# Kernel tuning notes

Hardware: AMD Instinct MI355X
Metric: run time of the kernel (lower is better)

## Reference

```python
import jax, jax.numpy as jnp
import numpy as np

EMB = 1024
HEADS = 16
EPS = 1e-6


def setup_inputs() -> dict:
    key = jax.random.key(0)
    ks = jax.random.split(key, 12)
    B, S, D = 2, 2048, EMB
    scale = 1.0 / np.sqrt(D)
    inp = {
        "v": jax.random.normal(ks[0], (B, S, D), jnp.float32),
        "k": jax.random.normal(ks[1], (B, S, D), jnp.float32),
        "q": jax.random.normal(ks[2], (B, S, D), jnp.float32),
        "Wv": jax.random.normal(ks[3], (D, D), jnp.float32) * scale,
        "bv": jnp.zeros((D,), jnp.float32),
        "Wk": jax.random.normal(ks[4], (D, D), jnp.float32) * scale,
        "bk": jnp.zeros((D,), jnp.float32),
        "Wq": jax.random.normal(ks[5], (D, D), jnp.float32) * scale,
        "bq": jnp.zeros((D,), jnp.float32),
        "Wo": jax.random.normal(ks[6], (D, D), jnp.float32) * scale,
        "bo": jnp.zeros((D,), jnp.float32),
        "gamma": jnp.ones((D,), jnp.float32),
        "beta": jnp.zeros((D,), jnp.float32),
    }
    return inp


def reference(v, k, q, Wv, bv, Wk, bk, Wq, bq, Wo, bo, gamma, beta):
    B, S, D = q.shape
    H = HEADS
    d = D // H  # head depth

    def split_heads(x):  # [B,S,D] -> [B,H,S,d]
        return x.reshape(B, S, H, d).transpose(0, 2, 1, 3)

    V = split_heads(v @ Wv + bv)
    K = split_heads(k @ Wk + bk)
    Q = split_heads(q @ Wq + bq)

    # scaled dot-product attention (full score matrix, no mask)
    scores = jnp.einsum("bhqd,bhkd->bhqk", Q, K) / jnp.sqrt(jnp.float32(d))
    attn = jax.nn.softmax(scores, axis=-1)
    ctx = jnp.einsum("bhqk,bhkd->bhqd", attn, V)

    ctx = ctx.transpose(0, 2, 1, 3).reshape(B, S, D)
    out = ctx @ Wo + bo + q  # final dense + residual

    # LayerNormalization(epsilon=1e-6) over last axis
    mu = jnp.mean(out, axis=-1, keepdims=True)
    var = jnp.var(out, axis=-1, keepdims=True)
    return gamma * (out - mu) * jax.lax.rsqrt(var + EPS) + beta
```

## Files before the change

kernel.cpp:

```cpp
#include <hip/hip_runtime.h>
#include <hip/hip_bf16.h>
#include <math.h>

#define D_EMB 1024
#define NBATCH 2
#define SEQ 2048
#define NH 16
#define HDIM 64
#define MTOT (NBATCH*SEQ)
#define NT (SEQ/64)

typedef unsigned short u16;
typedef __attribute__((ext_vector_type(8))) short bf16x8;
typedef __attribute__((ext_vector_type(4))) float f32x4;
typedef __attribute__((ext_vector_type(16))) float f32x16;
typedef __attribute__((ext_vector_type(4))) unsigned short u16x4;
typedef __attribute__((ext_vector_type(4))) unsigned int u32x4;

__device__ __forceinline__ u16 f2b(float f) {
  union { float f; unsigned u; } x; x.f = f;
  unsigned r = x.u + 0x7fffu + ((x.u >> 16) & 1u);
  return (u16)(r >> 16);
}
__device__ __forceinline__ float b2f(u16 u) {
  union { unsigned u; float f; } x; x.u = ((unsigned)u) << 16;
  return x.f;
}

__device__ __forceinline__ void gld_lds16(const u16* g, u16* l) {
  __builtin_amdgcn_global_load_lds(
      (const __attribute__((address_space(1))) void*)g,
      (__attribute__((address_space(3))) void*)l, 16, 0, 0);
}

__global__ __launch_bounds__(256) void convert_qkv(
    const float* __restrict__ v, const float* __restrict__ k, const float* __restrict__ q,
    u16* __restrict__ vb, u16* __restrict__ kb, u16* __restrict__ qb) {
  int idx = blockIdx.x * 256 + threadIdx.x;
  float4 a;
  u16x4 o;
  a = ((const float4*)v)[idx];
  o.x = f2b(a.x); o.y = f2b(a.y); o.z = f2b(a.z); o.w = f2b(a.w);
  ((u16x4*)vb)[idx] = o;
  a = ((const float4*)k)[idx];
  o.x = f2b(a.x); o.y = f2b(a.y); o.z = f2b(a.z); o.w = f2b(a.w);
  ((u16x4*)kb)[idx] = o;
  a = ((const float4*)q)[idx];
  o.x = f2b(a.x); o.y = f2b(a.y); o.z = f2b(a.z); o.w = f2b(a.w);
  ((u16x4*)qb)[idx] = o;
}

__global__ __launch_bounds__(256) void transpose_w(
    const float* __restrict__ Wv, const float* __restrict__ Wk,
    const float* __restrict__ Wq, const float* __restrict__ Wo,
    u16* __restrict__ Wvt, u16* __restrict__ Wkt,
    u16* __restrict__ Wqt, u16* __restrict__ Wot) {
  __shared__ float tile[32][33];
  int z = blockIdx.z;
  const float* W = (z==0) ? Wv : (z==1) ? Wk : (z==2) ? Wq : Wo;
  u16* Wt = (z==0) ? Wvt : (z==1) ? Wkt : (z==2) ? Wqt : Wot;
  int tx = threadIdx.x, ty = threadIdx.y;
  int n0 = blockIdx.x * 32, k0 = blockIdx.y * 32;
#pragma unroll
  for (int i = 0; i < 4; ++i)
    tile[ty + i*8][tx] = W[(size_t)(k0 + ty + i*8) * D_EMB + n0 + tx];
  __syncthreads();
#pragma unroll
  for (int i = 0; i < 4; ++i)
    Wt[(size_t)(n0 + ty + i*8) * D_EMB + k0 + tx] = f2b(tile[tx][ty + i*8]);
}

__global__ __launch_bounds__(256) void transpose_v(
    const u16* __restrict__ Vh, u16* __restrict__ Vt) {
  __shared__ u16 t[64][65];
  const int bhx = blockIdx.y, s0 = blockIdx.x * 64;
  const int tid = threadIdx.x;
  const u16* src = Vh + ((size_t)bhx * SEQ + s0) * HDIM;
  const int r = tid >> 3, seg = (tid & 7) * 8;
  bf16x8 a0 = *(const bf16x8*)(src + (size_t)r * HDIM + seg);
  bf16x8 a1 = *(const bf16x8*)(src + (size_t)(r + 32) * HDIM + seg);
#pragma unroll
  for (int j = 0; j < 8; ++j) {
    t[r][seg + j] = (u16)a0[j];
    t[r + 32][seg + j] = (u16)a1[j];
  }
  __syncthreads();
  const int dd = tid >> 3, ss = (tid & 7) * 8;
  bf16x8 w0, w1;
#pragma unroll
  for (int j = 0; j < 8; ++j) {
    w0[j] = (short)t[ss + j][dd];
    w1[j] = (short)t[ss + j][dd + 32];
  }
  *(bf16x8*)(Vt + ((size_t)bhx * HDIM + dd) * SEQ + s0 + ss) = w0;
  *(bf16x8*)(Vt + ((size_t)bhx * HDIM + dd + 32) * SEQ + s0 + ss) = w1;
}

__device__ __forceinline__ void gemm_loop(
    const u16* __restrict__ A, const u16* __restrict__ Bt,
    u16* lds_a, u16* lds_b, int bm, int bn, int wid, int lane,
    int wr, int wc, f32x4 acc[4][4]) {
#pragma unroll 1
  for (int kt = 0; kt < D_EMB/64; ++kt) {
    __syncthreads();
#pragma unroll
    for (int i = 0; i < 4; ++i) {
      int chunk = i*4 + wid;
      int row = chunk*8 + (lane >> 3);
      int slot = (lane & 7) ^ (row & 7);
      const u16* srcA = A + (size_t)(bm*128 + row) * D_EMB + kt*64 + slot*8;
      gld_lds16(srcA, lds_a + chunk*512);
      const u16* srcB = Bt + (size_t)(bn*128 + row) * D_EMB + kt*64 + slot*8;
      gld_lds16(srcB, lds_b + chunk*512);
    }
    __syncthreads();
#pragma unroll
    for (int st = 0; st < 2; ++st) {
      bf16x8 af[4], bfr[4];
#pragma unroll
      for (int mb = 0; mb < 4; ++mb) {
        int row = wr*64 + mb*16 + (lane & 15);
        int slot = (st*4 + (lane >> 4)) ^ (row & 7);
        af[mb] = *(const bf16x8*)(lds_a + row*64 + slot*8);
      }
#pragma unroll
      for (int nb = 0; nb < 4; ++nb) {
        int row = wc*64 + nb*16 + (lane & 15);
        int slot = (st*4 + (lane >> 4)) ^ (row & 7);
        bfr[nb] = *(const bf16x8*)(lds_b + row*64 + slot*8);
      }
#pragma unroll
      for (int mb = 0; mb < 4; ++mb)
#pragma unroll
        for (int nb = 0; nb < 4; ++nb)
          acc[mb][nb] = __builtin_amdgcn_mfma_f32_16x16x32_bf16(af[mb], bfr[nb], acc[mb][nb], 0, 0, 0);
    }
  }
}

__global__ __launch_bounds__(256) void gemm_qkv(
    const u16* __restrict__ vb, const u16* __restrict__ kb, const u16* __restrict__ qb,
    const u16* __restrict__ Wvt, const u16* __restrict__ Wkt, const u16* __restrict__ Wqt,
    const float* __restrict__ bv, const float* __restrict__ bk, const float* __restrict__ bq,
    u16* __restrict__ Vh, u16* __restrict__ Kh, u16* __restrict__ Qh) {
  __shared__ u16 lds_a[128*64];
  __shared__ u16 lds_b[128*64];
  int z = blockIdx.z;
  const u16* A  = (z==0) ? vb : (z==1) ? kb : qb;
  const u16* Bt = (z==0) ? Wvt : (z==1) ? Wkt : Wqt;
  const float* bias = (z==0) ? bv : (z==1) ? bk : bq;
  u16* Out = (z==0) ? Vh : (z==1) ? Kh : Qh;
  int tid = threadIdx.x, wid = tid >> 6, lane = tid & 63;
  int wr = wid >> 1, wc = wid & 1;
  int bm = blockIdx.y, bn = blockIdx.x;
  f32x4 acc[4][4];
#pragma unroll
  for (int i = 0; i < 4; ++i)
#pragma unroll
    for (int j = 0; j < 4; ++j) acc[i][j] = (f32x4){0.f,0.f,0.f,0.f};
  gemm_loop(A, Bt, lds_a, lds_b, bm, bn, wid, lane, wr, wc, acc);
  int g = lane >> 4, c = lane & 15;
  const float scl = (z == 2) ? 0.18033688f : 1.0f;
#pragma unroll
  for (int mb = 0; mb < 4; ++mb) {
    int row0 = bm*128 + wr*64 + mb*16 + g*4;
#pragma unroll
    for (int nb = 0; nb < 4; ++nb) {
      int col = bn*128 + wc*64 + nb*16 + c;
      float bsv = bias[col];
      int h = col >> 6, dd = col & 63;
#pragma unroll
      for (int r = 0; r < 4; ++r) {
        int m = row0 + r; int b = m >> 11, s = m & (SEQ-1);
        Out[(((size_t)b*NH + h)*SEQ + s)*HDIM + dd] = f2b((acc[mb][nb][r] + bsv) * scl);
      }
    }
  }
}

__global__ __launch_bounds__(256, 2) void attn_k(
    const u16* __restrict__ Qh, const u16* __restrict__ Kh,
    const u16* __restrict__ Vt, u16* __restrict__ ctx) {
  __shared__ u16 kt_lds[4][64*64];
  __shared__ u16 vt_lds[4][64*64];
  const int tid = threadIdx.x, wid = tid >> 6, lane = tid & 63;
  const int lo5 = lane & 31, hi = lane >> 5;
  const int bid = blockIdx.x;
  const int xcd = bid & 7, idx = bid >> 3;
  const int qblk = idx & 15, bhg = idx >> 4;
  const int bh = bhg * 8 + xcd;
  const int qb = qblk * 128 + wid * 32;
  const size_t base = (size_t)bh * SEQ * HDIM;

  const int srow = tid >> 3;
  const int c0 = (tid & 7) ^ (srow & 7) ^ (srow >> 3);
  const int c1 = c0 ^ 4;
  const u16* kp0 = Kh + base + (size_t)srow * HDIM + c0*8;
  const u16* kp1 = Kh + base + (size_t)(srow+32) * HDIM + c1*8;
  const u16* vp0 = Vt + base + (size_t)srow * SEQ + c0*8;
  const u16* vp1 = Vt + base + (size_t)(srow+32) * SEQ + c1*8;

  const int r7 = lo5 & 7, r3 = lo5 >> 3;
  int offs0[4], offs1[4];
#pragma unroll
  for (int t = 0; t < 4; ++t) {
    int p = (2*t + hi) ^ r7 ^ r3;
    offs0[t] = lo5*128 + p*16;
    offs1[t] = (lo5+32)*128 + (p^4)*16;
  }
  const char* ktbase = (const char*)&kt_lds[0][0];
  const char* vtbase = (const char*)&vt_lds[0][0];

  bf16x8 qf[4];
#pragma unroll
  for (int t = 0; t < 4; ++t)
    qf[t] = *(const bf16x8*)(Qh + base + (size_t)(qb + lo5)*HDIM + t*16 + hi*8);

  f32x16 z16;
#pragma unroll
  for (int i = 0; i < 16; ++i) z16[i] = 0.f;

  f32x16 o0, o1;
#pragma unroll
  for (int i = 0; i < 16; ++i) { o0[i] = 0.f; o1[i] = 0.f; }
  float lsum = 0.f;

#define STAGE(B) do { \
    gld_lds16(kp0, &kt_lds[B][wid*512]); \
    gld_lds16(kp1, &kt_lds[B][2048 + wid*512]); \
    gld_lds16(vp0, &vt_lds[B][wid*512]); \
    gld_lds16(vp1, &vt_lds[B][2048 + wid*512]); \
    kp0 += 64*HDIM; kp1 += 64*HDIM; vp0 += 64; vp1 += 64; \
  } while (0)

#define TILE(B, VMSTR, DOSTAGE, SB) do { \
    asm volatile("s_waitcnt " VMSTR ::: "memory"); \
    __builtin_amdgcn_sched_barrier(0); \
    __builtin_amdgcn_s_barrier();             \
    __builtin_amdgcn_sched_barrier(0); \
    const char* kb_ = ktbase + (B)*8192; \
    const char* vb_ = vtbase + (B)*8192; \
    bf16x8 kf0[4], kf1[4], vf0[4], vf1[4]; \
    _Pragma("unroll") for (int t = 0; t < 4; ++t) { \
      kf0[t] = *(const bf16x8*)(kb_ + offs0[t]); \
      kf1[t] = *(const bf16x8*)(kb_ + offs1[t]); \
      vf0[t] = *(const bf16x8*)(vb_ + offs0[t]); \
      vf1[t] = *(const bf16x8*)(vb_ + offs1[t]); } \
    if (DOSTAGE) { STAGE(SB); } \
    __builtin_amdgcn_sched_barrier(0); \
    __builtin_amdgcn_s_setprio(1); \
    f32x16 st0 = __builtin_amdgcn_mfma_f32_32x32x16_bf16(kf0[0], qf[0], z16, 0, 0, 0); \
    f32x16 st1 = __builtin_amdgcn_mfma_f32_32x32x16_bf16(kf1[0], qf[0], z16, 0, 0, 0); \
    _Pragma("unroll") for (int t = 1; t < 4; ++t) { \
      st0 = __builtin_amdgcn_mfma_f32_32x32x16_bf16(kf0[t], qf[t], st0, 0, 0, 0); \
      st1 = __builtin_amdgcn_mfma_f32_32x32x16_bf16(kf1[t], qf[t], st1, 0, 0, 0); } \
    __builtin_amdgcn_s_setprio(0); \
    _Pragma("unroll") for (int r = 0; r < 16; ++r) { \
      st0[r] = exp2f(st0[r]); st1[r] = exp2f(st1[r]); } \
    float ps = st0[0] + st0[1]; \
    _Pragma("unroll") for (int r = 2; r < 16; ++r) ps += st0[r]; \
    _Pragma("unroll") for (int r = 0; r < 16; ++r) ps += st1[r]; \
    lsum += ps; \
    bf16x8 pa[4]; \
    _Pragma("unroll") for (int ks = 0; ks < 2; ++ks) { \
      const f32x16& s_ = ks ? st1 : st0; \
      unsigned X[8]; \
      _Pragma("unroll") for (int w = 0; w < 8; ++w) { \
        float lo_f = s_[2*w], hi_f = s_[2*w + 1]; \
        asm("v_cvt_pk_bf16_f32 %0, %1, %2" : "=v"(X[w]) : "v"(lo_f), "v"(hi_f)); } \
      asm volatile("v_permlane32_swap_b32 %0, %1" : "+v"(X[0]), "+v"(X[2])); \
      asm volatile("v_permlane32_swap_b32 %0, %1" : "+v"(X[1]), "+v"(X[3])); \
      asm volatile("v_permlane32_swap_b32 %0, %1" : "+v"(X[4]), "+v"(X[6])); \
      asm volatile("v_permlane32_swap_b32 %0, %1" : "+v"(X[5]), "+v"(X[7])); \
      union { u32x4 u; bf16x8 b; } cva, cvb; \
      cva.u = (u32x4){X[0], X[1], X[2], X[3]}; \
      cvb.u = (u32x4){X[4], X[5], X[6], X[7]}; \
      pa[2*ks]   = cva.b; \
      pa[2*ks+1] = cvb.b; } \
    __builtin_amdgcn_s_setprio(1); \
    _Pragma("unroll") for (int t = 0; t < 4; ++t) { \
      o0 = __builtin_amdgcn_mfma_f32_32x32x16_bf16(pa[t], vf0[t], o0, 0, 0, 0); \
      o1 = __builtin_amdgcn_mfma_f32_32x32x16_bf16(pa[t], vf1[t], o1, 0, 0, 0); } \
    __builtin_amdgcn_s_setprio(0); \
  } while (0)

  STAGE(0);
  STAGE(1);

#pragma unroll 1
  for (int kv = 0; kv < NT - 4; kv += 4) {
    TILE(0, "vmcnt(4)", 1, 2);
    TILE(1, "vmcnt(4)", 1, 3);
    TILE(2, "vmcnt(4)", 1, 0);
    TILE(3, "vmcnt(4)", 1, 1);
  }
  TILE(0, "vmcnt(4)", 1, 2);
  TILE(1, "vmcnt(4)", 1, 3);
  TILE(2, "vmcnt(4)", 0, 0);
  TILE(3, "vmcnt(0)", 0, 0);

#undef STAGE
#undef TILE

  lsum += __shfl_xor(lsum, 32);
  float linv = 1.0f / lsum;
  const int b = bh >> 4, h = bh & 15;
#pragma unroll
  for (int r = 0; r < 16; ++r) {
    int crow = (r & 3) + 8*(r >> 2) + 4*hi;
    float lr = __int_as_float(
        __builtin_amdgcn_ds_bpermute(crow << 2, __float_as_int(linv)));
    int s = qb + crow;
    u16* row = ctx + ((size_t)(b*SEQ + s))*D_EMB + h*64;
    row[lo5]      = f2b(o0[r] * lr);
    row[32 + lo5] = f2b(o1[r] * lr);
  }
}

__global__ __launch_bounds__(256) void gemm_out(
    const u16* __restrict__ ctx, const u16* __restrict__ Wot,
    const float* __restrict__ bo, const u16* __restrict__ resid,
    u16* __restrict__ preln) {
  __shared__ u16 lds_a[128*64];
  __shared__ u16 lds_b[128*64];
  int tid = threadIdx.x, wid = tid >> 6, lane = tid & 63;
  int wr = wid >> 1, wc = wid & 1;
  int bm = blockIdx.y, bn = blockIdx.x;
  f32x4 acc[4][4];
#pragma unroll
  for (int i = 0; i < 4; ++i)
#pragma unroll
    for (int j = 0; j < 4; ++j) acc[i][j] = (f32x4){0.f,0.f,0.f,0.f};
  gemm_loop(ctx, Wot, lds_a, lds_b, bm, bn, wid, lane, wr, wc, acc);
  int g = lane >> 4, c = lane & 15;
#pragma unroll
  for (int mb = 0; mb < 4; ++mb) {
    int row0 = bm*128 + wr*64 + mb*16 + g*4;
#pragma unroll
    for (int nb = 0; nb < 4; ++nb) {
      int col = bn*128 + wc*64 + nb*16 + c;
      float bsv = bo[col];
#pragma unroll
      for (int r = 0; r < 4; ++r) {
        int m = row0 + r;
        float v = acc[mb][nb][r] + bsv + b2f(resid[(size_t)m*D_EMB + col]);
        preln[(size_t)m*D_EMB + col] = f2b(v);
      }
    }
  }
}

__global__ __launch_bounds__(256) void ln_k(
    const u16* __restrict__ preln, const float* __restrict__ gamma,
    const float* __restrict__ beta, float* __restrict__ out) {
  int row = blockIdx.x, tid = threadIdx.x;
  u16x4 xr = ((const u16x4*)(preln + (size_t)row*D_EMB))[tid];
  float x0 = b2f(xr.x), x1 = b2f(xr.y), x2 = b2f(xr.z), x3 = b2f(xr.w);
  float s  = x0 + x1 + x2 + x3;
  float ss = x0*x0 + x1*x1 + x2*x2 + x3*x3;
#pragma unroll
  for (int off = 32; off; off >>= 1) {
    s  += __shfl_xor(s, off);
    ss += __shfl_xor(ss, off);
  }
  __shared__ float red_s[4], red_ss[4];
  int wid = tid >> 6, lane = tid & 63;
  if (lane == 0) { red_s[wid] = s; red_ss[wid] = ss; }
  __syncthreads();
  s  = red_s[0] + red_s[1] + red_s[2] + red_s[3];
  ss = red_ss[0] + red_ss[1] + red_ss[2] + red_ss[3];
  float mu = s * (1.0f/1024.0f);
  float var = ss * (1.0f/1024.0f) - mu*mu;
  float rstd = rsqrtf(var + 1e-6f);
  float4 gm = ((const float4*)gamma)[tid];
  float4 bt = ((const float4*)beta)[tid];
  float4 y;
  y.x = (x0 - mu)*rstd*gm.x + bt.x;
  y.y = (x1 - mu)*rstd*gm.y + bt.y;
  y.z = (x2 - mu)*rstd*gm.z + bt.z;
  y.w = (x3 - mu)*rstd*gm.w + bt.w;
  ((float4*)(out + (size_t)row*D_EMB))[tid] = y;
}

extern "C" void kernel_launch(void* const* d_in, const int* in_sizes, int n_in,
                              void* d_out, int out_size, void* d_ws, size_t ws_size,
                              hipStream_t stream) {
  const float* v_in  = (const float*)d_in[0];
  const float* k_in  = (const float*)d_in[1];
  const float* q_in  = (const float*)d_in[2];
  const float* Wv    = (const float*)d_in[3];
  const float* bv    = (const float*)d_in[4];
  const float* Wk    = (const float*)d_in[5];
  const float* bk    = (const float*)d_in[6];
  const float* Wq    = (const float*)d_in[7];
  const float* bq    = (const float*)d_in[8];
  const float* Wo    = (const float*)d_in[9];
  const float* bo    = (const float*)d_in[10];
  const float* gamma = (const float*)d_in[11];
  const float* beta  = (const float*)d_in[12];
  char* ws = (char*)d_ws;

  const size_t TOKB = (size_t)MTOT * D_EMB * 2;
  const size_t WB   = (size_t)D_EMB * D_EMB * 2;
  size_t o_qb = 0;
  size_t o_kb = o_qb + TOKB;
  size_t o_vb = o_kb + TOKB;
  size_t o_wq = o_vb + TOKB;
  size_t o_wk = o_wq + WB;
  size_t o_wv = o_wk + WB;
  size_t o_wo = o_wv + WB;
  size_t o_Qh = o_wo + WB;
  size_t o_Kh = o_Qh + TOKB;
  size_t o_Vt = o_Kh + TOKB;
  size_t o_cx = o_Vt + TOKB;

  u16* qb  = (u16*)(ws + o_qb);
  u16* kb  = (u16*)(ws + o_kb);
  u16* vb  = (u16*)(ws + o_vb);
  u16* wqt = (u16*)(ws + o_wq);
  u16* wkt = (u16*)(ws + o_wk);
  u16* wvt = (u16*)(ws + o_wv);
  u16* wot = (u16*)(ws + o_wo);
  u16* Qh  = (u16*)(ws + o_Qh);
  u16* Kh  = (u16*)(ws + o_Kh);
  u16* Vt  = (u16*)(ws + o_Vt);
  u16* cx  = (u16*)(ws + o_cx);
  u16* Vh  = cx;
  u16* preln = vb;

  convert_qkv<<<4096, 256, 0, stream>>>(v_in, k_in, q_in, vb, kb, qb);
  transpose_w<<<dim3(32, 32, 4), dim3(32, 8), 0, stream>>>(Wv, Wk, Wq, Wo, wvt, wkt, wqt, wot);
  gemm_qkv<<<dim3(8, 32, 3), 256, 0, stream>>>(vb, kb, qb, wvt, wkt, wqt, bv, bk, bq, Vh, Kh, Qh);
  transpose_v<<<dim3(32, 32), 256, 0, stream>>>(Vh, Vt);
  attn_k<<<512, 256, 0, stream>>>(Qh, Kh, Vt, cx);
  gemm_out<<<dim3(8, 32), 256, 0, stream>>>(cx, wot, bo, qb, preln);
  ln_k<<<4096, 256, 0, stream>>>(preln, gamma, beta, (float*)d_out);
}
```

Before: 155.4 us.

## Shrink GEMM M-tile to 64 rows and double-buffer attention K/V staging

The QKV and output projection GEMMs now use 64x128 block tiles instead of 128x128, which doubles the grid (8x64 blocks) to fill more compute units, at the cost of less operand reuse per block. The attention kernel's K/V LDS ring shrinks from four buffers to two. A second barrier after each tile's LDS reads lets the next tile's prefetch overwrite the same buffer. This halves LDS use, which may help occupancy, but it adds a barrier per tile and leaves less prefetch depth to hide memory latency.

```diff
diff --git a/kernel.cpp b/kernel.cpp
--- a/kernel.cpp
+++ b/kernel.cpp
@@ -96,43 +96,49 @@
   *(bf16x8*)(Vt + ((size_t)bhx * HDIM + dd + 32) * SEQ + s0 + ss) = w1;
 }
 
-__device__ __forceinline__ void gemm_loop(
+__device__ __forceinline__ void gemm_loop64(
     const u16* __restrict__ A, const u16* __restrict__ Bt,
     u16* lds_a, u16* lds_b, int bm, int bn, int wid, int lane,
-    int wr, int wc, f32x4 acc[4][4]) {
+    f32x4 acc[4][2]) {
 #pragma unroll 1
   for (int kt = 0; kt < D_EMB/64; ++kt) {
     __syncthreads();
+#pragma unroll
+    for (int i = 0; i < 2; ++i) {
+      int chunk = wid*2 + i;
+      int row = chunk*8 + (lane >> 3);
+      int slot = (lane & 7) ^ (row & 7);
+      gld_lds16(A + (size_t)(bm*64 + row) * D_EMB + kt*64 + slot*8,
+                lds_a + chunk*512);
+    }
 #pragma unroll
     for (int i = 0; i < 4; ++i) {
       int chunk = i*4 + wid;
       int row = chunk*8 + (lane >> 3);
       int slot = (lane & 7) ^ (row & 7);
-      const u16* srcA = A + (size_t)(bm*128 + row) * D_EMB + kt*64 + slot*8;
-      gld_lds16(srcA, lds_a + chunk*512);
-      const u16* srcB = Bt + (size_t)(bn*128 + row) * D_EMB + kt*64 + slot*8;
-      gld_lds16(srcB, lds_b + chunk*512);
+      gld_lds16(Bt + (size_t)(bn*128 + row) * D_EMB + kt*64 + slot*8,
+                lds_b + chunk*512);
     }
     __syncthreads();
 #pragma unroll
     for (int st = 0; st < 2; ++st) {
-      bf16x8 af[4], bfr[4];
+      bf16x8 af[4], bfr[2];
 #pragma unroll
       for (int mb = 0; mb < 4; ++mb) {
-        int row = wr*64 + mb*16 + (lane & 15);
+        int row = mb*16 + (lane & 15);
         int slot = (st*4 + (lane >> 4)) ^ (row & 7);
         af[mb] = *(const bf16x8*)(lds_a + row*64 + slot*8);
       }
 #pragma unroll
-      for (int nb = 0; nb < 4; ++nb) {
-        int row = wc*64 + nb*16 + (lane & 15);
+      for (int nb = 0; nb < 2; ++nb) {
+        int row = wid*32 + nb*16 + (lane & 15);
         int slot = (st*4 + (lane >> 4)) ^ (row & 7);
         bfr[nb] = *(const bf16x8*)(lds_b + row*64 + slot*8);
       }
 #pragma unroll
       for (int mb = 0; mb < 4; ++mb)
 #pragma unroll
-        for (int nb = 0; nb < 4; ++nb)
+        for (int nb = 0; nb < 2; ++nb)
           acc[mb][nb] = __builtin_amdgcn_mfma_f32_16x16x32_bf16(af[mb], bfr[nb], acc[mb][nb], 0, 0, 0);
     }
   }
@@ -143,7 +149,7 @@
     const u16* __restrict__ Wvt, const u16* __restrict__ Wkt, const u16* __restrict__ Wqt,
     const float* __restrict__ bv, const float* __restrict__ bk, const float* __restrict__ bq,
     u16* __restrict__ Vh, u16* __restrict__ Kh, u16* __restrict__ Qh) {
-  __shared__ u16 lds_a[128*64];
+  __shared__ u16 lds_a[64*64];
   __shared__ u16 lds_b[128*64];
   int z = blockIdx.z;
   const u16* A  = (z==0) ? vb : (z==1) ? kb : qb;
@@ -151,22 +157,21 @@
   const float* bias = (z==0) ? bv : (z==1) ? bk : bq;
   u16* Out = (z==0) ? Vh : (z==1) ? Kh : Qh;
   int tid = threadIdx.x, wid = tid >> 6, lane = tid & 63;
-  int wr = wid >> 1, wc = wid & 1;
   int bm = blockIdx.y, bn = blockIdx.x;
-  f32x4 acc[4][4];
+  f32x4 acc[4][2];
 #pragma unroll
   for (int i = 0; i < 4; ++i)
 #pragma unroll
-    for (int j = 0; j < 4; ++j) acc[i][j] = (f32x4){0.f,0.f,0.f,0.f};
-  gemm_loop(A, Bt, lds_a, lds_b, bm, bn, wid, lane, wr, wc, acc);
+    for (int j = 0; j < 2; ++j) acc[i][j] = (f32x4){0.f,0.f,0.f,0.f};
+  gemm_loop64(A, Bt, lds_a, lds_b, bm, bn, wid, lane, acc);
   int g = lane >> 4, c = lane & 15;
   const float scl = (z == 2) ? 0.18033688f : 1.0f;
 #pragma unroll
   for (int mb = 0; mb < 4; ++mb) {
-    int row0 = bm*128 + wr*64 + mb*16 + g*4;
-#pragma unroll
-    for (int nb = 0; nb < 4; ++nb) {
-      int col = bn*128 + wc*64 + nb*16 + c;
+    int row0 = bm*64 + mb*16 + g*4;
+#pragma unroll
+    for (int nb = 0; nb < 2; ++nb) {
+      int col = bn*128 + wid*32 + nb*16 + c;
       float bsv = bias[col];
       int h = col >> 6, dd = col & 63;
 #pragma unroll
@@ -181,8 +186,8 @@
 __global__ __launch_bounds__(256, 2) void attn_k(
     const u16* __restrict__ Qh, const u16* __restrict__ Kh,
     const u16* __restrict__ Vt, u16* __restrict__ ctx) {
-  __shared__ u16 kt_lds[4][64*64];
-  __shared__ u16 vt_lds[4][64*64];
+  __shared__ u16 kt_lds[2][64*64];
+  __shared__ u16 vt_lds[2][64*64];
   const int tid = threadIdx.x, wid = tid >> 6, lane = tid & 63;
   const int lo5 = lane & 31, hi = lane >> 5;
   const int bid = blockIdx.x;
@@ -233,7 +238,7 @@
     kp0 += 64*HDIM; kp1 += 64*HDIM; vp0 += 64; vp1 += 64; \
   } while (0)
 
-#define TILE(B, VMSTR, DOSTAGE, SB) do { \
+#define TILE(B, VMSTR, DOSTAGE) do { \
     asm volatile("s_waitcnt " VMSTR ::: "memory"); \
     __builtin_amdgcn_sched_barrier(0); \
     __builtin_amdgcn_s_barrier();             \
@@ -246,7 +251,11 @@
       kf1[t] = *(const bf16x8*)(kb_ + offs1[t]); \
       vf0[t] = *(const bf16x8*)(vb_ + offs0[t]); \
       vf1[t] = *(const bf16x8*)(vb_ + offs1[t]); } \
-    if (DOSTAGE) { STAGE(SB); } \
+    asm volatile("s_waitcnt lgkmcnt(0)" ::: "memory"); \
+    __builtin_amdgcn_sched_barrier(0); \
+    __builtin_amdgcn_s_barrier();             \
+    __builtin_amdgcn_sched_barrier(0); \
+    if (DOSTAGE) { STAGE(B); } \
     __builtin_amdgcn_sched_barrier(0); \
     __builtin_amdgcn_s_setprio(1); \
     f32x16 st0 = __builtin_amdgcn_mfma_f32_32x32x16_bf16(kf0[0], qf[0], z16, 0, 0, 0); \
@@ -288,16 +297,12 @@
   STAGE(1);
 
 #pragma unroll 1
-  for (int kv = 0; kv < NT - 4; kv += 4) {
-    TILE(0, "vmcnt(4)", 1, 2);
-    TILE(1, "vmcnt(4)", 1, 3);
-    TILE(2, "vmcnt(4)", 1, 0);
-    TILE(3, "vmcnt(4)", 1, 1);
-  }
-  TILE(0, "vmcnt(4)", 1, 2);
-  TILE(1, "vmcnt(4)", 1, 3);
-  TILE(2, "vmcnt(4)", 0, 0);
-  TILE(3, "vmcnt(0)", 0, 0);
+  for (int kv = 0; kv < NT - 2; kv += 2) {
+    TILE(0, "vmcnt(4)", 1);
+    TILE(1, "vmcnt(4)", 1);
+  }
+  TILE(0, "vmcnt(4)", 0);
+  TILE(1, "vmcnt(0)", 0);
 
 #undef STAGE
 #undef TILE
@@ -321,24 +326,23 @@
     const u16* __restrict__ ctx, const u16* __restrict__ Wot,
     const float* __restrict__ bo, const u16* __restrict__ resid,
     u16* __restrict__ preln) {
-  __shared__ u16 lds_a[128*64];
+  __shared__ u16 lds_a[64*64];
   __shared__ u16 lds_b[128*64];
   int tid = threadIdx.x, wid = tid >> 6, lane = tid & 63;
-  int wr = wid >> 1, wc = wid & 1;
   int bm = blockIdx.y, bn = blockIdx.x;
-  f32x4 acc[4][4];
+  f32x4 acc[4][2];
 #pragma unroll
   for (int i = 0; i < 4; ++i)
 #pragma unroll
-    for (int j = 0; j < 4; ++j) acc[i][j] = (f32x4){0.f,0.f,0.f,0.f};
-  gemm_loop(ctx, Wot, lds_a, lds_b, bm, bn, wid, lane, wr, wc, acc);
+    for (int j = 0; j < 2; ++j) acc[i][j] = (f32x4){0.f,0.f,0.f,0.f};
+  gemm_loop64(ctx, Wot, lds_a, lds_b, bm, bn, wid, lane, acc);
   int g = lane >> 4, c = lane & 15;
 #pragma unroll
   for (int mb = 0; mb < 4; ++mb) {
-    int row0 = bm*128 + wr*64 + mb*16 + g*4;
-#pragma unroll
-    for (int nb = 0; nb < 4; ++nb) {
-      int col = bn*128 + wc*64 + nb*16 + c;
+    int row0 = bm*64 + mb*16 + g*4;
+#pragma unroll
+    for (int nb = 0; nb < 2; ++nb) {
+      int col = bn*128 + wid*32 + nb*16 + c;
       float bsv = bo[col];
 #pragma unroll
       for (int r = 0; r < 4; ++r) {
@@ -430,9 +434,9 @@
 
   convert_qkv<<<4096, 256, 0, stream>>>(v_in, k_in, q_in, vb, kb, qb);
   transpose_w<<<dim3(32, 32, 4), dim3(32, 8), 0, stream>>>(Wv, Wk, Wq, Wo, wvt, wkt, wqt, wot);
-  gemm_qkv<<<dim3(8, 32, 3), 256, 0, stream>>>(vb, kb, qb, wvt, wkt, wqt, bv, bk, bq, Vh, Kh, Qh);
+  gemm_qkv<<<dim3(8, 64, 3), 256, 0, stream>>>(vb, kb, qb, wvt, wkt, wqt, bv, bk, bq, Vh, Kh, Qh);
   transpose_v<<<dim3(32, 32), 256, 0, stream>>>(Vh, Vt);
   attn_k<<<512, 256, 0, stream>>>(Qh, Kh, Vt, cx);
-  gemm_out<<<dim3(8, 32), 256, 0, stream>>>(cx, wot, bo, qb, preln);
+  gemm_out<<<dim3(8, 64), 256, 0, stream>>>(cx, wot, bo, qb, preln);
   ln_k<<<4096, 256, 0, stream>>>(preln, gamma, beta, (float*)d_out);
 }
```

Result: faster. 150.2 us (-3.3%).
